# Kernel tuning notes

Hardware: AMD Instinct MI355X
Metric: run time of the kernel (lower is better)

The kernel has to match this reference:

```python
import jax, jax.numpy as jnp
import numpy as np

D_MODEL = 768
H = 12
D_K = D_MODEL // H
B = 2
S = 2048
NEG = -1e9


def setup_inputs() -> dict:
    key = jax.random.key(0)
    ks = jax.random.split(key, 12)
    scale = 1.0 / np.sqrt(D_MODEL)
    inp = {
        "q": jax.random.normal(ks[0], (B, S, D_MODEL), jnp.float32),
        "k": jax.random.normal(ks[1], (B, S, D_MODEL), jnp.float32),
        "v": jax.random.normal(ks[2], (B, S, D_MODEL), jnp.float32),
        "mask": jax.random.randint(ks[3], (B, 1, S, S), 0, 2, jnp.int32),
        "Wq": jax.random.normal(ks[4], (D_MODEL, D_MODEL), jnp.float32) * scale,
        "bq": jnp.zeros((D_MODEL,), jnp.float32),
        "Wk": jax.random.normal(ks[5], (D_MODEL, D_MODEL), jnp.float32) * scale,
        "bk": jnp.zeros((D_MODEL,), jnp.float32),
        "Wv": jax.random.normal(ks[6], (D_MODEL, D_MODEL), jnp.float32) * scale,
        "bv": jnp.zeros((D_MODEL,), jnp.float32),
        "Wo": jax.random.normal(ks[7], (D_MODEL, D_MODEL), jnp.float32) * scale,
        "bo": jnp.zeros((D_MODEL,), jnp.float32),
    }
    return inp


def _split_heads(x):
    # [B, S, D] -> [B, H, S, D_K]
    b, s, _ = x.shape
    return x.reshape(b, s, H, D_K).transpose(0, 2, 1, 3)


def reference(q, k, v, mask, Wq, bq, Wk, bk, Wv, bv, Wo, bo):
    # torch Linear: x @ W.T + b
    query = _split_heads(q @ Wq.T + bq)
    key_ = _split_heads(k @ Wk.T + bk)
    value = _split_heads(v @ Wv.T + bv)

    scores = jnp.einsum("bhqd,bhkd->bhqk", query, key_) / np.sqrt(D_K)
    scores = jnp.where(mask == 0, NEG, scores)
    attn = jax.nn.softmax(scores, axis=-1)  # dropout p=0.0 -> identity

    x = jnp.einsum("bhqk,bhkd->bhqd", attn, value)
    x = x.transpose(0, 2, 1, 3).reshape(q.shape[0], -1, D_MODEL)
    return x @ Wo.T + bo
```

## Files before the change

kernel.cpp:

```cpp
#include <hip/hip_runtime.h>
#include <math.h>

#define DMODEL 768
#define NHEAD 12
#define DKDIM 64
#define BB 2
#define SS 2048
#define MROWS (BB * SS)
#define WELEM (DMODEL * DMODEL)
#define MWORDS (SS / 64)

typedef unsigned short bf16_t;
typedef __attribute__((ext_vector_type(8))) short s8;
typedef __attribute__((ext_vector_type(4))) float f4;

#define MFMA(a, b, c) __builtin_amdgcn_mfma_f32_16x16x32_bf16((a), (b), (c), 0, 0, 0)

__device__ __forceinline__ bf16_t f2bf(float f) {
    unsigned u = __float_as_uint(f);
    u += 0x7fffu + ((u >> 16) & 1u);
    return (bf16_t)(u >> 16);
}
__device__ __forceinline__ unsigned pack2(float a, float b) {
    return (unsigned)f2bf(a) | ((unsigned)f2bf(b) << 16);
}
__device__ __forceinline__ s8 ldfrag(const bf16_t* p) {
    union { uint4 u; s8 s; } x;
    x.u = *(const uint4*)p;
    return x.s;
}

__device__ __forceinline__ void ld_stage(const bf16_t* p, uint4& u0, uint4& u1) {
    u0 = *(const uint4*)p;
    u1 = *(const uint4*)(p + 8);
}
__device__ __forceinline__ void ld_stage(const float* p, uint4& u0, uint4& u1) {
    const float4 f0 = *(const float4*)p;
    const float4 f1 = *(const float4*)(p + 4);
    const float4 f2 = *(const float4*)(p + 8);
    const float4 f3 = *(const float4*)(p + 12);
    u0.x = pack2(f0.x, f0.y); u0.y = pack2(f0.z, f0.w);
    u0.z = pack2(f1.x, f1.y); u0.w = pack2(f1.z, f1.w);
    u1.x = pack2(f2.x, f2.y); u1.y = pack2(f2.z, f2.w);
    u1.z = pack2(f3.x, f3.y); u1.w = pack2(f3.z, f3.w);
}

__global__ void cvt_weights(const float* __restrict__ W0, const float* __restrict__ W1,
                            const float* __restrict__ W2, const float* __restrict__ W3,
                            bf16_t* __restrict__ dst)
{
    const float* src = (blockIdx.y == 0) ? W0 : (blockIdx.y == 1) ? W1
                     : (blockIdx.y == 2) ? W2 : W3;
    bf16_t* d = dst + (size_t)blockIdx.y * WELEM;
    const int i = (blockIdx.x * 256 + threadIdx.x) * 4;
    const float4 v = *(const float4*)(src + i);
    ushort4 h;
    h.x = f2bf(v.x); h.y = f2bf(v.y); h.z = f2bf(v.z); h.w = f2bf(v.w);
    *(ushort4*)(d + i) = h;
}

__global__ __launch_bounds__(256) void mask_to_bits(
    const int* __restrict__ mask, unsigned long long* __restrict__ mbits)
{
    const size_t gid = (size_t)blockIdx.x * 256 + threadIdx.x;
    const int m = mask[gid];
    const unsigned long long bal = __ballot(m != 0);
    if ((threadIdx.x & 63) == 0) mbits[gid >> 6] = bal;
}

template<typename TA, typename TO>
__global__ __launch_bounds__(256) void gemm_tiled(
    const TA* __restrict__ A0, const TA* __restrict__ A1, const TA* __restrict__ A2,
    const bf16_t* __restrict__ W0, const bf16_t* __restrict__ W1, const bf16_t* __restrict__ W2,
    const float* __restrict__ bias0, const float* __restrict__ bias1, const float* __restrict__ bias2,
    TO* __restrict__ C0, TO* __restrict__ C1, TO* __restrict__ C2,
    float sc0, float sc1, float sc2)
{
    __shared__ uint4 As4[128 * 4];
    __shared__ uint4 Bs4[128 * 4];

    const int z = blockIdx.z;
    const TA*     A    = (z == 0) ? A0 : (z == 1) ? A1 : A2;
    const bf16_t* W    = (z == 0) ? W0 : (z == 1) ? W1 : W2;
    const float*  bias = (z == 0) ? bias0 : (z == 1) ? bias1 : bias2;
    TO*           C    = (z == 0) ? C0 : (z == 1) ? C1 : C2;
    const float   sc   = (z == 0) ? sc0 : (z == 1) ? sc1 : sc2;

    const int tid  = threadIdx.x;
    const int lane = tid & 63;
    const int w    = tid >> 6;
    const int wm   = w & 1;
    const int wn   = w >> 1;
    const int l15  = lane & 15;
    const int quad = lane >> 4;
    const int m0   = blockIdx.y * 128;
    const int n0   = blockIdx.x * 128;

    const int srow  = tid >> 1;
    const int shalf = tid & 1;
    const int sw    = srow & 3;

    const TA*     aptr = A + (size_t)(m0 + srow) * DMODEL + shalf * 16;
    const bf16_t* wptr = W + (size_t)(n0 + srow) * DMODEL + shalf * 16;

    f4 acc[4][4];
    #pragma unroll
    for (int i = 0; i < 4; i++)
        #pragma unroll
        for (int j = 0; j < 4; j++)
            acc[i][j] = (f4){0.f, 0.f, 0.f, 0.f};

    for (int k0 = 0; k0 < DMODEL; k0 += 32) {
        uint4 au0, au1, bu0, bu1;
        ld_stage(aptr + k0, au0, au1);
        ld_stage(wptr + k0, bu0, bu1);
        __syncthreads();
        As4[srow * 4 + ((shalf * 2 + 0) ^ sw)] = au0;
        As4[srow * 4 + ((shalf * 2 + 1) ^ sw)] = au1;
        Bs4[srow * 4 + ((shalf * 2 + 0) ^ sw)] = bu0;
        Bs4[srow * 4 + ((shalf * 2 + 1) ^ sw)] = bu1;
        __syncthreads();

        s8 af[4], bf[4];
        #pragma unroll
        for (int t = 0; t < 4; t++) {
            const int ar = wm * 64 + t * 16 + l15;
            const int br = wn * 64 + t * 16 + l15;
            union { uint4 u; s8 s; } xa, xb;
            xa.u = As4[ar * 4 + (quad ^ (ar & 3))];
            xb.u = Bs4[br * 4 + (quad ^ (br & 3))];
            af[t] = xa.s;
            bf[t] = xb.s;
        }
        #pragma unroll
        for (int mt = 0; mt < 4; mt++)
            #pragma unroll
            for (int nt = 0; nt < 4; nt++)
                acc[mt][nt] = MFMA(af[mt], bf[nt], acc[mt][nt]);
    }

    #pragma unroll
    for (int mt = 0; mt < 4; mt++) {
        #pragma unroll
        for (int nt = 0; nt < 4; nt++) {
            const int col = n0 + wn * 64 + nt * 16 + l15;
            const float bb = bias[col];
            #pragma unroll
            for (int reg = 0; reg < 4; reg++) {
                const int row = m0 + wm * 64 + mt * 16 + quad * 4 + reg;
                const float val = (acc[mt][nt][reg] + bb) * sc;
                TO* dst = C + (size_t)row * DMODEL + col;
                if constexpr (sizeof(TO) == 2) *dst = f2bf(val);
                else                           *dst = val;
            }
        }
    }
}

__global__ __launch_bounds__(256) void attn_mfma(
    const bf16_t* __restrict__ Q, const bf16_t* __restrict__ K,
    const bf16_t* __restrict__ V, const unsigned long long* __restrict__ mbits,
    bf16_t* __restrict__ O)
{
    __shared__ unsigned Vs[2][64][36];
    __shared__ unsigned Ps[4][16][36];

    const int tid  = threadIdx.x;
    const int lane = tid & 63;
    const int w    = tid >> 6;
    const int l15  = lane & 15;
    const int quad = lane >> 4;
    const int q0   = blockIdx.x * 64;
    const int h    = blockIdx.y;
    const int b    = blockIdx.z;
    const size_t base = ((size_t)b * SS) * DMODEL + (size_t)h * DKDIM;

    const bf16_t* qrow = Q + base + (size_t)(q0 + w * 16 + l15) * DMODEL + quad * 8;
    const s8 qf0 = ldfrag(qrow);
    const s8 qf1 = ldfrag(qrow + 32);

    f4 oacc[4];
    float l_part[4];
    #pragma unroll
    for (int i = 0; i < 4; i++) {
        oacc[i] = (f4){0.f, 0.f, 0.f, 0.f};
        l_part[i] = 0.0f;
    }

    const int kp  = tid & 31;
    const int oct = tid >> 5;
    const bf16_t* vbase = V + base + (size_t)(2 * kp) * DMODEL + oct * 8;

    const unsigned long long* mbase =
        mbits + ((size_t)b * SS + (q0 + w * 16 + quad * 4)) * MWORDS;

    uint4 va = *(const uint4*)(vbase);
    uint4 vb = *(const uint4*)(vbase + DMODEL);
    {
        const unsigned short* pa = (const unsigned short*)&va;
        const unsigned short* pb = (const unsigned short*)&vb;
        #pragma unroll
        for (int i = 0; i < 8; i++)
            Vs[0][oct * 8 + i][kp] = (unsigned)pa[i] | ((unsigned)pb[i] << 16);
    }
    va = *(const uint4*)(vbase + (size_t)64 * DMODEL);
    vb = *(const uint4*)(vbase + (size_t)64 * DMODEL + DMODEL);
    __syncthreads();

    for (int it = 0; it < SS / 64; ++it) {
        const int k0  = it * 64;
        const int cur = it & 1;

        if (it + 1 < SS / 64) {
            const unsigned short* pa = (const unsigned short*)&va;
            const unsigned short* pb = (const unsigned short*)&vb;
            #pragma unroll
            for (int i = 0; i < 8; i++)
                Vs[cur ^ 1][oct * 8 + i][kp] = (unsigned)pa[i] | ((unsigned)pb[i] << 16);
            if (it + 2 < SS / 64) {
                va = *(const uint4*)(vbase + (size_t)(k0 + 128) * DMODEL);
                vb = *(const uint4*)(vbase + (size_t)(k0 + 128) * DMODEL + DMODEL);
            }
        }

        unsigned long long mw[4];
        #pragma unroll
        for (int reg = 0; reg < 4; reg++)
            mw[reg] = mbase[(size_t)reg * MWORDS + it];

        f4 sacc[4];
        #pragma unroll
        for (int nt = 0; nt < 4; nt++) {
            const bf16_t* krow = K + base + (size_t)(k0 + nt * 16 + l15) * DMODEL + quad * 8;
            f4 zz = {0.f, 0.f, 0.f, 0.f};
            zz = MFMA(qf0, ldfrag(krow), zz);
            zz = MFMA(qf1, ldfrag(krow + 32), zz);
            sacc[nt] = zz;
        }

        #pragma unroll
        for (int reg = 0; reg < 4; reg++) {
            const unsigned mlo = ((unsigned)mw[reg]) >> l15;
            const unsigned mhi = ((unsigned)(mw[reg] >> 32)) >> l15;
            float p[4];
            p[0] = (mlo & 1u)       ? __expf(sacc[0][reg]) : 0.0f;
            p[1] = (mlo & 0x10000u) ? __expf(sacc[1][reg]) : 0.0f;
            p[2] = (mhi & 1u)       ? __expf(sacc[2][reg]) : 0.0f;
            p[3] = (mhi & 0x10000u) ? __expf(sacc[3][reg]) : 0.0f;
            l_part[reg] += (p[0] + p[1]) + (p[2] + p[3]);

            #pragma unroll
            for (int nt = 0; nt < 4; nt++) {
                const float mine  = p[nt];
                const float other = __shfl_xor(mine, 1, 16);
                if ((lane & 1) == 0)
                    Ps[w][quad * 4 + reg][nt * 8 + (l15 >> 1)] = pack2(mine, other);
            }
        }

        #pragma unroll
        for (int kt = 0; kt < 2; kt++) {
            union { uint4 u; s8 s; } pf;
            pf.u = *(const uint4*)&Ps[w][l15][kt * 16 + quad * 4];
            #pragma unroll
            for (int dt = 0; dt < 4; dt++) {
                union { uint4 u; s8 s; } vf;
                vf.u = *(const uint4*)&Vs[cur][dt * 16 + l15][kt * 16 + quad * 4];
                oacc[dt] = MFMA(pf.s, vf.s, oacc[dt]);
            }
        }

        __syncthreads();
    }

    #pragma unroll
    for (int reg = 0; reg < 4; reg++) {
        float rs = l_part[reg];
        rs += __shfl_xor(rs, 1, 16);
        rs += __shfl_xor(rs, 2, 16);
        rs += __shfl_xor(rs, 4, 16);
        rs += __shfl_xor(rs, 8, 16);
        const float inv = 1.0f / rs;
        const size_t row = q0 + w * 16 + quad * 4 + reg;
        #pragma unroll
        for (int dt = 0; dt < 4; dt++) {
            O[base + row * DMODEL + dt * 16 + l15] = f2bf(oacc[dt][reg] * inv);
        }
    }
}

extern "C" void kernel_launch(void* const* d_in, const int* in_sizes, int n_in,
                              void* d_out, int out_size, void* d_ws, size_t ws_size,
                              hipStream_t stream)
{
    const float* q    = (const float*)d_in[0];
    const float* k    = (const float*)d_in[1];
    const float* v    = (const float*)d_in[2];
    const int*   mask = (const int*)  d_in[3];
    const float* Wq   = (const float*)d_in[4];
    const float* bq   = (const float*)d_in[5];
    const float* Wk   = (const float*)d_in[6];
    const float* bk   = (const float*)d_in[7];
    const float* Wv   = (const float*)d_in[8];
    const float* bv   = (const float*)d_in[9];
    const float* Wo   = (const float*)d_in[10];
    const float* bo   = (const float*)d_in[11];
    float* out = (float*)d_out;

    bf16_t* wsb = (bf16_t*)d_ws;
    const size_t plane = (size_t)MROWS * DMODEL;
    bf16_t* Qp  = wsb;
    bf16_t* Kp  = wsb + plane;
    bf16_t* Vp  = wsb + 2 * plane;
    bf16_t* Ctx = wsb + 3 * plane;
    bf16_t* Wqb = wsb + 4 * plane;
    bf16_t* Wkb = Wqb + WELEM;
    bf16_t* Wvb = Wkb + WELEM;
    bf16_t* Wob = Wvb + WELEM;
    unsigned long long* mbits = (unsigned long long*)(Wob + WELEM);

    cvt_weights<<<dim3(WELEM / 1024, 4), 256, 0, stream>>>(Wq, Wk, Wv, Wo, Wqb);
    mask_to_bits<<<dim3((BB * SS * SS) / 256), 256, 0, stream>>>(mask, mbits);

    gemm_tiled<float, bf16_t><<<dim3(DMODEL / 128, MROWS / 128, 3), 256, 0, stream>>>(
        q, k, v, Wqb, Wkb, Wvb, bq, bk, bv, Qp, Kp, Vp, 0.125f, 1.0f, 1.0f);

    attn_mfma<<<dim3(SS / 64, NHEAD, BB), 256, 0, stream>>>(Qp, Kp, Vp, mbits, Ctx);

    gemm_tiled<bf16_t, float><<<dim3(DMODEL / 128, MROWS / 128, 1), 256, 0, stream>>>(
        Ctx, Ctx, Ctx, Wob, Wob, Wob, bo, bo, bo, out, out, out, 1.0f, 1.0f, 1.0f);
}
```

Baseline: 335.7 us.

## Prefetch K fragments and mask words one iteration ahead, use hardware bf16 pack

```diff
diff --git a/kernel.cpp b/kernel.cpp
--- a/kernel.cpp
+++ b/kernel.cpp
@@ -9,6 +9,7 @@
 #define MROWS (BB * SS)
 #define WELEM (DMODEL * DMODEL)
 #define MWORDS (SS / 64)
+#define NIT (SS / 64)
 
 typedef unsigned short bf16_t;
 typedef __attribute__((ext_vector_type(8))) short s8;
@@ -21,8 +22,10 @@
     u += 0x7fffu + ((u >> 16) & 1u);
     return (bf16_t)(u >> 16);
 }
-__device__ __forceinline__ unsigned pack2(float a, float b) {
-    return (unsigned)f2bf(a) | ((unsigned)f2bf(b) << 16);
+__device__ __forceinline__ unsigned cvtpk2(float a, float b) {
+    unsigned r;
+    asm("v_cvt_pk_bf16_f32 %0, %1, %2" : "=v"(r) : "v"(a), "v"(b));
+    return r;
 }
 __device__ __forceinline__ s8 ldfrag(const bf16_t* p) {
     union { uint4 u; s8 s; } x;
@@ -39,10 +42,10 @@
     const float4 f1 = *(const float4*)(p + 4);
     const float4 f2 = *(const float4*)(p + 8);
     const float4 f3 = *(const float4*)(p + 12);
-    u0.x = pack2(f0.x, f0.y); u0.y = pack2(f0.z, f0.w);
-    u0.z = pack2(f1.x, f1.y); u0.w = pack2(f1.z, f1.w);
-    u1.x = pack2(f2.x, f2.y); u1.y = pack2(f2.z, f2.w);
-    u1.z = pack2(f3.x, f3.y); u1.w = pack2(f3.z, f3.w);
+    u0.x = cvtpk2(f0.x, f0.y); u0.y = cvtpk2(f0.z, f0.w);
+    u0.z = cvtpk2(f1.x, f1.y); u0.w = cvtpk2(f1.z, f1.w);
+    u1.x = cvtpk2(f2.x, f2.y); u1.y = cvtpk2(f2.z, f2.w);
+    u1.z = cvtpk2(f3.x, f3.y); u1.w = cvtpk2(f3.z, f3.w);
 }
 
 __global__ void cvt_weights(const float* __restrict__ W0, const float* __restrict__ W1,
@@ -54,9 +57,10 @@
     bf16_t* d = dst + (size_t)blockIdx.y * WELEM;
     const int i = (blockIdx.x * 256 + threadIdx.x) * 4;
     const float4 v = *(const float4*)(src + i);
-    ushort4 h;
-    h.x = f2bf(v.x); h.y = f2bf(v.y); h.z = f2bf(v.z); h.w = f2bf(v.w);
-    *(ushort4*)(d + i) = h;
+    uint2 h;
+    h.x = cvtpk2(v.x, v.y);
+    h.y = cvtpk2(v.z, v.w);
+    *(uint2*)(d + i) = h;
 }
 
 __global__ __launch_bounds__(256) void mask_to_bits(
@@ -190,6 +194,7 @@
     const int kp  = tid & 31;
     const int oct = tid >> 5;
     const bf16_t* vbase = V + base + (size_t)(2 * kp) * DMODEL + oct * 8;
+    const bf16_t* kbase = K + base + (size_t)l15 * DMODEL + quad * 8;
 
     const unsigned long long* mbase =
         mbits + ((size_t)b * SS + (q0 + w * 16 + quad * 4)) * MWORDS;
@@ -205,43 +210,67 @@
     }
     va = *(const uint4*)(vbase + (size_t)64 * DMODEL);
     vb = *(const uint4*)(vbase + (size_t)64 * DMODEL + DMODEL);
+
+    s8 kf0[4], kf1[4];
+    unsigned long long mw[4];
+    #pragma unroll
+    for (int nt = 0; nt < 4; nt++) {
+        const bf16_t* krow = kbase + (size_t)(nt * 16) * DMODEL;
+        kf0[nt] = ldfrag(krow);
+        kf1[nt] = ldfrag(krow + 32);
+    }
+    #pragma unroll
+    for (int reg = 0; reg < 4; reg++)
+        mw[reg] = mbase[(size_t)reg * MWORDS];
+
     __syncthreads();
 
-    for (int it = 0; it < SS / 64; ++it) {
+    for (int it = 0; it < NIT; ++it) {
         const int k0  = it * 64;
         const int cur = it & 1;
 
-        if (it + 1 < SS / 64) {
+        if (it + 1 < NIT) {
             const unsigned short* pa = (const unsigned short*)&va;
             const unsigned short* pb = (const unsigned short*)&vb;
             #pragma unroll
             for (int i = 0; i < 8; i++)
                 Vs[cur ^ 1][oct * 8 + i][kp] = (unsigned)pa[i] | ((unsigned)pb[i] << 16);
-            if (it + 2 < SS / 64) {
+            if (it + 2 < NIT) {
                 va = *(const uint4*)(vbase + (size_t)(k0 + 128) * DMODEL);
                 vb = *(const uint4*)(vbase + (size_t)(k0 + 128) * DMODEL + DMODEL);
             }
         }
 
-        unsigned long long mw[4];
-        #pragma unroll
-        for (int reg = 0; reg < 4; reg++)
-            mw[reg] = mbase[(size_t)reg * MWORDS + it];
-
         f4 sacc[4];
+        __builtin_amdgcn_s_setprio(1);
         #pragma unroll
         for (int nt = 0; nt < 4; nt++) {
-            const bf16_t* krow = K + base + (size_t)(k0 + nt * 16 + l15) * DMODEL + quad * 8;
             f4 zz = {0.f, 0.f, 0.f, 0.f};
-            zz = MFMA(qf0, ldfrag(krow), zz);
-            zz = MFMA(qf1, ldfrag(krow + 32), zz);
+            zz = MFMA(qf0, kf0[nt], zz);
+            zz = MFMA(qf1, kf1[nt], zz);
             sacc[nt] = zz;
         }
+        __builtin_amdgcn_s_setprio(0);
+
+        unsigned long long mwc[4];
+        #pragma unroll
+        for (int reg = 0; reg < 4; reg++) mwc[reg] = mw[reg];
+        if (it + 1 < NIT) {
+            #pragma unroll
+            for (int nt = 0; nt < 4; nt++) {
+                const bf16_t* krow = kbase + (size_t)(k0 + 64 + nt * 16) * DMODEL;
+                kf0[nt] = ldfrag(krow);
+                kf1[nt] = ldfrag(krow + 32);
+            }
+            #pragma unroll
+            for (int reg = 0; reg < 4; reg++)
+                mw[reg] = mbase[(size_t)reg * MWORDS + it + 1];
+        }
 
         #pragma unroll
         for (int reg = 0; reg < 4; reg++) {
-            const unsigned mlo = ((unsigned)mw[reg]) >> l15;
-            const unsigned mhi = ((unsigned)(mw[reg] >> 32)) >> l15;
+            const unsigned mlo = ((unsigned)mwc[reg]) >> l15;
+            const unsigned mhi = ((unsigned)(mwc[reg] >> 32)) >> l15;
             float p[4];
             p[0] = (mlo & 1u)       ? __expf(sacc[0][reg]) : 0.0f;
             p[1] = (mlo & 0x10000u) ? __expf(sacc[1][reg]) : 0.0f;
@@ -254,10 +283,11 @@
                 const float mine  = p[nt];
                 const float other = __shfl_xor(mine, 1, 16);
                 if ((lane & 1) == 0)
-                    Ps[w][quad * 4 + reg][nt * 8 + (l15 >> 1)] = pack2(mine, other);
-            }
-        }
-
+                    Ps[w][quad * 4 + reg][nt * 8 + (l15 >> 1)] = cvtpk2(mine, other);
+            }
+        }
+
+        __builtin_amdgcn_s_setprio(1);
         #pragma unroll
         for (int kt = 0; kt < 2; kt++) {
             union { uint4 u; s8 s; } pf;
@@ -269,6 +299,7 @@
                 oacc[dt] = MFMA(pf.s, vf.s, oacc[dt]);
             }
         }
+        __builtin_amdgcn_s_setprio(0);
 
         __syncthreads();
     }
```

Measured after the change: 340.6 us. About the same (+1.5%).
